# Kernel optimization log

Measured on AMD Instinct MI355X. Metric: run time of the kernel, lower is better.

The kernel has to match this reference:

```python
import jax, jax.numpy as jnp
import numpy as np
from jax.scipy.linalg import expm

B, T, N_IN, N_HID, N_OUT = 8192, 2048, 2, 10, 10


def setup_inputs() -> dict:
    key = jax.random.key(0)
    k0, k1, k2, k3, k4 = jax.random.split(key, 5)
    inputs = jax.random.normal(k0, (B, T, N_IN), dtype=jnp.float32)
    # skew-symmetric seed for the orthogonal recurrent kernel (expm parametrization)
    A = jax.random.normal(k1, (N_HID, N_HID), dtype=jnp.float32) * 0.1
    # input_kernel: nn.Linear(n_inputs, n_hidden, bias=False) -> weight [H, D_in]
    W_in = jax.random.normal(k2, (N_HID, N_IN), dtype=jnp.float32) / np.sqrt(N_IN)
    # modrelu bias, initialized uniform(-0.01, 0.01) as in exprnn
    b_mod = jax.random.uniform(k3, (N_HID,), jnp.float32, -0.01, 0.01)
    # final nn.Linear(n_hidden, n_outputs)
    lin_W = jax.random.normal(k4, (N_OUT, N_HID), dtype=jnp.float32) / np.sqrt(N_HID)
    lin_b = jnp.zeros((N_OUT,), jnp.float32)
    return {"inputs": inputs, "A": A, "W_in": W_in, "b_mod": b_mod,
            "lin_W": lin_W, "lin_b": lin_b}


def _modrelu(z, b):
    # modrelu(z) = sign(z) * relu(|z| + b)
    return jnp.sign(z) * jax.nn.relu(jnp.abs(z) + b)


def reference(inputs, A, W_in, b_mod, lin_W, lin_b):
    # Orthogonal recurrent matrix: Bmat = expm(skew(A)), skew from strict upper triangle
    A_tri = jnp.triu(A, k=1)
    Bmat = expm(A_tri - A_tri.T)  # [H, H], orthogonal
    # Precompute input projections for all timesteps: [B, T, H]
    x_proj = jnp.einsum('btd,hd->bth', inputs, W_in)
    h0 = jnp.zeros((inputs.shape[0], W_in.shape[0]), dtype=inputs.dtype)

    def step(h, x_t):
        h_new = _modrelu(x_t + h @ Bmat, b_mod)
        return h_new, None

    hT, _ = jax.lax.scan(step, h0, jnp.swapaxes(x_proj, 0, 1))  # scan over time
    out = hT @ lin_W.T + lin_b  # [B, n_outputs]
    return out
```

## Files before the change

kernel.cpp:

```cpp
#include <hip/hip_runtime.h>

#define H 10
#define T_LEN 2048
#define BATCH 8192

#define MOVROR(x, K) __int_as_float(__builtin_amdgcn_mov_dpp(                    \
    __float_as_int(x), 0x120 + (K), 0xF, 0xF, true))

__global__ void expm_kernel(const float* __restrict__ A, float* __restrict__ Bout) {
    __shared__ double S[H][H];
    __shared__ double P[H][H];
    __shared__ double E[H][H];
    const int tid = threadIdx.x;
    const int i = tid / H, j = tid % H;
    if (tid < H * H) {
        double a = 0.0;
        if (i < j) a = (double)A[i * H + j];
        else if (i > j) a = -(double)A[j * H + i];
        a *= (1.0 / 256.0);
        S[i][j] = a;
        P[i][j] = a;
        E[i][j] = (i == j ? 1.0 : 0.0) + a;
    }
    __syncthreads();
    for (int k = 2; k <= 16; ++k) {
        double acc = 0.0;
        if (tid < H * H) {
            for (int m = 0; m < H; ++m) acc += P[i][m] * S[m][j];
            acc *= (1.0 / (double)k);
        }
        __syncthreads();
        if (tid < H * H) { P[i][j] = acc; E[i][j] += acc; }
        __syncthreads();
    }
    for (int rr = 0; rr < 8; ++rr) {
        double acc = 0.0;
        if (tid < H * H) {
            for (int m = 0; m < H; ++m) acc += E[i][m] * E[m][j];
        }
        __syncthreads();
        if (tid < H * H) E[i][j] = acc;
        __syncthreads();
    }
    if (tid < H * H) Bout[i * H + j] = (float)E[i][j];
}

__global__ __launch_bounds__(64)
void rnn_kernel(const float* __restrict__ x,
                const float* __restrict__ Bm,
                const float* __restrict__ Win,
                const float* __restrict__ bmod,
                const float* __restrict__ lW,
                const float* __restrict__ lb,
                float* __restrict__ out) {
    const int lane = threadIdx.x;
    const int j    = lane & 15;
    const int row  = lane >> 4;
    const int bb   = blockIdx.x * 4 + row;

    float Brot[16];
#pragma unroll
    for (int k = 0; k < 16; ++k) {
        const int m = (j - k) & 15;
        Brot[k] = (j < H && m < H) ? Bm[m * H + j] : 0.f;
    }
    float w0j = 0.f, w1j = 0.f, bmj = 0.f;
    if (j < H) { w0j = Win[j * 2]; w1j = Win[j * 2 + 1]; bmj = bmod[j]; }

    float h = 0.f;

    const float4* __restrict__ xp4 = (const float4*)(x + (size_t)bb * (T_LEN * 2));
    float4 buf[8];
#pragma unroll
    for (int i = 0; i < 8; ++i) buf[i] = xp4[i];

    for (int t0 = 0; t0 < T_LEN; t0 += 16) {
        float4 c[8];
#pragma unroll
        for (int i = 0; i < 8; ++i) c[i] = buf[i];
        if (t0 + 16 < T_LEN) {
            const int base = (t0 + 16) >> 1;
#pragma unroll
            for (int i = 0; i < 8; ++i) buf[i] = xp4[base + i];
        }

#pragma unroll
        for (int u = 0; u < 16; ++u) {
            const int ii = u >> 1;
            const float x0 = (u & 1) ? c[ii].z : c[ii].x;
            const float x1 = (u & 1) ? c[ii].w : c[ii].y;

            float acc = fmaf(x1, w1j, x0 * w0j);
            acc = fmaf(h, Brot[0], acc);
#define STEPK(K) { const float e_ = MOVROR(h, K); acc = fmaf(e_, Brot[K], acc); }
            STEPK(1)  STEPK(2)  STEPK(3)  STEPK(4)  STEPK(5)
            STEPK(6)  STEPK(7)  STEPK(8)  STEPK(9)  STEPK(10)
            STEPK(11) STEPK(12) STEPK(13) STEPK(14) STEPK(15)
#undef STEPK
            const float s = acc;
            const float r = fmaxf(fabsf(s) + bmj, 0.f);
            h = __builtin_copysignf(r, s);
        }
    }

    float Lrot[16];
#pragma unroll
    for (int k = 0; k < 16; ++k) {
        const int m = (j - k) & 15;
        Lrot[k] = (j < H && m < H) ? lW[j * H + m] : 0.f;
    }
    float acc = (j < H) ? lb[j] : 0.f;
    acc = fmaf(h, Lrot[0], acc);
#define OUTK(K) { const float e_ = MOVROR(h, K); acc = fmaf(e_, Lrot[K], acc); }
    OUTK(1)  OUTK(2)  OUTK(3)  OUTK(4)  OUTK(5)
    OUTK(6)  OUTK(7)  OUTK(8)  OUTK(9)  OUTK(10)
    OUTK(11) OUTK(12) OUTK(13) OUTK(14) OUTK(15)
#undef OUTK
    if (j < H) out[(size_t)bb * H + j] = acc;
}

extern "C" void kernel_launch(void* const* d_in, const int* in_sizes, int n_in,
                              void* d_out, int out_size, void* d_ws, size_t ws_size,
                              hipStream_t stream) {
    const float* inputs = (const float*)d_in[0];
    const float* A      = (const float*)d_in[1];
    const float* W_in   = (const float*)d_in[2];
    const float* b_mod  = (const float*)d_in[3];
    const float* lin_W  = (const float*)d_in[4];
    const float* lin_b  = (const float*)d_in[5];
    float* out = (float*)d_out;
    float* Bmat = (float*)d_ws;

    expm_kernel<<<1, 128, 0, stream>>>(A, Bmat);
    rnn_kernel<<<BATCH / 4, 64, 0, stream>>>(inputs, Bmat, W_in, b_mod,
                                             lin_W, lin_b, out);
}
```

Baseline: 389.5 us.

## Fold DPP row rotations into v_fmac via inline asm and double-buffer input loads

Replaces each separate DPP mov plus FMA with a single v_fmac_f32 carrying a row_ror DPP modifier, written in inline asm. This roughly halves the instruction count on the serial recurrence critical path. Input prefetch now uses two ping-pong register buffers over 32 timesteps, which removes the buffer copy. Launch bounds gain a minimum of 2 blocks. The s_nop before the first DPP op covers the VALU-write-to-DPP-read hazard, but inline asm hides these dependencies from the compiler's hazard tracking and scheduling.

```diff
diff --git a/kernel.cpp b/kernel.cpp
--- a/kernel.cpp
+++ b/kernel.cpp
@@ -6,6 +6,14 @@
 
 #define MOVROR(x, K) __int_as_float(__builtin_amdgcn_mov_dpp(                    \
     __float_as_int(x), 0x120 + (K), 0xF, 0xF, true))
+
+#define STR_(x) #x
+#define FMAC_ROR(acc, hh, bk, K)                                                  \
+    asm("v_fmac_f32 %0, %1, %2 row_ror:" STR_(K) " row_mask:0xf bank_mask:0xf"    \
+        : "+v"(acc) : "v"(hh), "v"(bk))
+#define FMAC_ROR1(acc, hh, bk)                                                    \
+    asm("s_nop 1\n\tv_fmac_f32 %0, %1, %2 row_ror:1 row_mask:0xf bank_mask:0xf"   \
+        : "+v"(acc) : "v"(hh), "v"(bk))
 
 __global__ void expm_kernel(const float* __restrict__ A, float* __restrict__ Bout) {
     __shared__ double S[H][H];
@@ -45,7 +53,47 @@
     if (tid < H * H) Bout[i * H + j] = (float)E[i][j];
 }
 
-__global__ __launch_bounds__(64)
+struct RnnConsts {
+    float w0j, w1j, bmj;
+};
+
+__device__ __forceinline__ void rnn_step(float x0, float x1, float& h,
+                                         const float (&Brot)[16],
+                                         const RnnConsts& cst) {
+    float acc = fmaf(x1, cst.w1j, x0 * cst.w0j);
+    acc = fmaf(h, Brot[0], acc);
+    FMAC_ROR1(acc, h, Brot[1]);
+    FMAC_ROR(acc, h, Brot[2],  2);
+    FMAC_ROR(acc, h, Brot[3],  3);
+    FMAC_ROR(acc, h, Brot[4],  4);
+    FMAC_ROR(acc, h, Brot[5],  5);
+    FMAC_ROR(acc, h, Brot[6],  6);
+    FMAC_ROR(acc, h, Brot[7],  7);
+    FMAC_ROR(acc, h, Brot[8],  8);
+    FMAC_ROR(acc, h, Brot[9],  9);
+    FMAC_ROR(acc, h, Brot[10], 10);
+    FMAC_ROR(acc, h, Brot[11], 11);
+    FMAC_ROR(acc, h, Brot[12], 12);
+    FMAC_ROR(acc, h, Brot[13], 13);
+    FMAC_ROR(acc, h, Brot[14], 14);
+    FMAC_ROR(acc, h, Brot[15], 15);
+    const float r = fmaxf(fabsf(acc) + cst.bmj, 0.f);
+    h = __builtin_copysignf(r, acc);
+}
+
+__device__ __forceinline__ void run16(const float4 (&c)[8], float& h,
+                                      const float (&Brot)[16],
+                                      const RnnConsts& cst) {
+#pragma unroll
+    for (int u = 0; u < 16; ++u) {
+        const int ii = u >> 1;
+        const float x0 = (u & 1) ? c[ii].z : c[ii].x;
+        const float x1 = (u & 1) ? c[ii].w : c[ii].y;
+        rnn_step(x0, x1, h, Brot, cst);
+    }
+}
+
+__global__ __launch_bounds__(64, 2)
 void rnn_kernel(const float* __restrict__ x,
                 const float* __restrict__ Bm,
                 const float* __restrict__ Win,
@@ -64,43 +112,27 @@
         const int m = (j - k) & 15;
         Brot[k] = (j < H && m < H) ? Bm[m * H + j] : 0.f;
     }
-    float w0j = 0.f, w1j = 0.f, bmj = 0.f;
-    if (j < H) { w0j = Win[j * 2]; w1j = Win[j * 2 + 1]; bmj = bmod[j]; }
+    RnnConsts cst = {0.f, 0.f, 0.f};
+    if (j < H) { cst.w0j = Win[j * 2]; cst.w1j = Win[j * 2 + 1]; cst.bmj = bmod[j]; }
 
     float h = 0.f;
 
     const float4* __restrict__ xp4 = (const float4*)(x + (size_t)bb * (T_LEN * 2));
-    float4 buf[8];
+    float4 bA[8], bB[8];
 #pragma unroll
-    for (int i = 0; i < 8; ++i) buf[i] = xp4[i];
+    for (int i = 0; i < 8; ++i) bA[i] = xp4[i];
 
-    for (int t0 = 0; t0 < T_LEN; t0 += 16) {
-        float4 c[8];
+    for (int t0 = 0; t0 < T_LEN; t0 += 32) {
+        const int baseB = (t0 + 16) >> 1;
 #pragma unroll
-        for (int i = 0; i < 8; ++i) c[i] = buf[i];
-        if (t0 + 16 < T_LEN) {
-            const int base = (t0 + 16) >> 1;
+        for (int i = 0; i < 8; ++i) bB[i] = xp4[baseB + i];
+        run16(bA, h, Brot, cst);
+        if (t0 + 32 < T_LEN) {
+            const int baseA = (t0 + 32) >> 1;
 #pragma unroll
-            for (int i = 0; i < 8; ++i) buf[i] = xp4[base + i];
+            for (int i = 0; i < 8; ++i) bA[i] = xp4[baseA + i];
         }
-
-#pragma unroll
-        for (int u = 0; u < 16; ++u) {
-            const int ii = u >> 1;
-            const float x0 = (u & 1) ? c[ii].z : c[ii].x;
-            const float x1 = (u & 1) ? c[ii].w : c[ii].y;
-
-            float acc = fmaf(x1, w1j, x0 * w0j);
-            acc = fmaf(h, Brot[0], acc);
-#define STEPK(K) { const float e_ = MOVROR(h, K); acc = fmaf(e_, Brot[K], acc); }
-            STEPK(1)  STEPK(2)  STEPK(3)  STEPK(4)  STEPK(5)
-            STEPK(6)  STEPK(7)  STEPK(8)  STEPK(9)  STEPK(10)
-            STEPK(11) STEPK(12) STEPK(13) STEPK(14) STEPK(15)
-#undef STEPK
-            const float s = acc;
-            const float r = fmaxf(fabsf(s) + bmj, 0.f);
-            h = __builtin_copysignf(r, s);
-        }
+        run16(bB, h, Brot, cst);
     }
 
     float Lrot[16];
```

New measurement: 345.4 us. 11.3% less time.

## Hand-write RNN recurrence in inline asm with DPP-fused FMAs and split accumulators

Applied to the files above, without the earlier changes.

Replaces the compiled time loop with inline assembly that folds the row-rotate DPP into each v_fmac and splits the 16-term dot product into two interleaved accumulator chains. The two chains are summed before modReLU, which is done with bit masking and v_bfi. Input loads use a four-stage rotating register buffer with manual vmcnt waits to overlap memory with the serial recurrence. This targets per-step latency on the dependent chain, but hard-codes VGPRs v60-v127 and adds launch_bounds occupancy 2, so register pressure may limit other code.

```diff
diff --git a/kernel.cpp b/kernel.cpp
--- a/kernel.cpp
+++ b/kernel.cpp
@@ -6,6 +6,51 @@
 
 #define MOVROR(x, K) __int_as_float(__builtin_amdgcn_mov_dpp(                    \
     __float_as_int(x), 0x120 + (K), 0xF, 0xF, true))
+
+#define STR2(x) #x
+#define VREG(n) "v" STR2(n)
+#define DPP_(K) " row_ror:" STR2(K) " row_mask:0xf bank_mask:0xf\n\t"
+
+#define STEP(X0, X1)                                                \
+    "v_mul_f32 v62, " VREG(X0) ", %[w0]\n\t"                        \
+    "v_fmac_f32 v62, " VREG(X1) ", %[w1]\n\t"                       \
+    "v_fmac_f32 v62, %[h], %[b0]\n\t"                               \
+    "v_mul_f32 v63, %[h], %[b8]" DPP_(8)                            \
+    "v_fmac_f32 v62, %[h], %[b1]" DPP_(1)                           \
+    "v_fmac_f32 v63, %[h], %[b9]" DPP_(9)                           \
+    "v_fmac_f32 v62, %[h], %[b2]" DPP_(2)                           \
+    "v_fmac_f32 v63, %[h], %[b10]" DPP_(10)                         \
+    "v_fmac_f32 v62, %[h], %[b3]" DPP_(3)                           \
+    "v_fmac_f32 v63, %[h], %[b11]" DPP_(11)                         \
+    "v_fmac_f32 v62, %[h], %[b4]" DPP_(4)                           \
+    "v_fmac_f32 v63, %[h], %[b12]" DPP_(12)                         \
+    "v_fmac_f32 v62, %[h], %[b5]" DPP_(5)                           \
+    "v_fmac_f32 v63, %[h], %[b13]" DPP_(13)                         \
+    "v_fmac_f32 v62, %[h], %[b6]" DPP_(6)                           \
+    "v_fmac_f32 v63, %[h], %[b14]" DPP_(14)                         \
+    "v_fmac_f32 v62, %[h], %[b7]" DPP_(7)                           \
+    "v_fmac_f32 v63, %[h], %[b15]" DPP_(15)                         \
+    "v_add_f32 v62, v62, v63\n\t"                                   \
+    "v_and_b32 v63, %[mk], v62\n\t"                                 \
+    "v_add_f32 v63, v63, %[bm]\n\t"                                 \
+    "v_max_f32 v63, 0, v63\n\t"                                     \
+    "v_bfi_b32 %[h], %[mk], v63, v62\n\t"
+
+#define SUBCTL(TAG, LD0, LD1, LD2, LD3)                             \
+    "s_cmp_lt_u32 %[it], 253\n\t"                                   \
+    "s_cbranch_scc0 Lsk" TAG "_%=\n\t"                              \
+    "global_load_dwordx4 " LD0 ", v[60:61], off\n\t"                \
+    "global_load_dwordx4 " LD1 ", v[60:61], off offset:16\n\t"      \
+    "global_load_dwordx4 " LD2 ", v[60:61], off offset:32\n\t"      \
+    "global_load_dwordx4 " LD3 ", v[60:61], off offset:48\n\t"      \
+    "v_add_co_u32 v60, vcc, 64, v60\n\t"                            \
+    "v_addc_co_u32 v61, vcc, 0, v61, vcc\n\t"                       \
+    "s_waitcnt vmcnt(12)\n\t"                                       \
+    "s_branch Ldn" TAG "_%=\n\t"                                    \
+    "Lsk" TAG "_%=:\n\t"                                            \
+    "s_waitcnt vmcnt(0)\n\t"                                        \
+    "Ldn" TAG "_%=:\n\t"                                            \
+    "s_add_i32 %[it], %[it], 1\n\t"
 
 __global__ void expm_kernel(const float* __restrict__ A, float* __restrict__ Bout) {
     __shared__ double S[H][H];
@@ -45,7 +90,7 @@
     if (tid < H * H) Bout[i * H + j] = (float)E[i][j];
 }
 
-__global__ __launch_bounds__(64)
+__global__ __launch_bounds__(64, 2)
 void rnn_kernel(const float* __restrict__ x,
                 const float* __restrict__ Bm,
                 const float* __restrict__ Win,
@@ -58,50 +103,69 @@
     const int row  = lane >> 4;
     const int bb   = blockIdx.x * 4 + row;
 
-    float Brot[16];
+    float Bv[16];
 #pragma unroll
     for (int k = 0; k < 16; ++k) {
         const int m = (j - k) & 15;
-        Brot[k] = (j < H && m < H) ? Bm[m * H + j] : 0.f;
+        Bv[k] = (j < H && m < H) ? Bm[m * H + j] : 0.f;
     }
     float w0j = 0.f, w1j = 0.f, bmj = 0.f;
     if (j < H) { w0j = Win[j * 2]; w1j = Win[j * 2 + 1]; bmj = bmod[j]; }
 
     float h = 0.f;
-
-    const float4* __restrict__ xp4 = (const float4*)(x + (size_t)bb * (T_LEN * 2));
-    float4 buf[8];
-#pragma unroll
-    for (int i = 0; i < 8; ++i) buf[i] = xp4[i];
-
-    for (int t0 = 0; t0 < T_LEN; t0 += 16) {
-        float4 c[8];
-#pragma unroll
-        for (int i = 0; i < 8; ++i) c[i] = buf[i];
-        if (t0 + 16 < T_LEN) {
-            const int base = (t0 + 16) >> 1;
-#pragma unroll
-            for (int i = 0; i < 8; ++i) buf[i] = xp4[base + i];
-        }
-
-#pragma unroll
-        for (int u = 0; u < 16; ++u) {
-            const int ii = u >> 1;
-            const float x0 = (u & 1) ? c[ii].z : c[ii].x;
-            const float x1 = (u & 1) ? c[ii].w : c[ii].y;
-
-            float acc = fmaf(x1, w1j, x0 * w0j);
-            acc = fmaf(h, Brot[0], acc);
-#define STEPK(K) { const float e_ = MOVROR(h, K); acc = fmaf(e_, Brot[K], acc); }
-            STEPK(1)  STEPK(2)  STEPK(3)  STEPK(4)  STEPK(5)
-            STEPK(6)  STEPK(7)  STEPK(8)  STEPK(9)  STEPK(10)
-            STEPK(11) STEPK(12) STEPK(13) STEPK(14) STEPK(15)
-#undef STEPK
-            const float s = acc;
-            const float r = fmaxf(fabsf(s) + bmj, 0.f);
-            h = __builtin_copysignf(r, s);
-        }
-    }
+    int it = 0;
+    const uint64_t addr = (uint64_t)(x + (size_t)bb * (T_LEN * 2));
+    const unsigned alo = (unsigned)addr, ahi = (unsigned)(addr >> 32);
+
+    asm volatile(
+        "v_mov_b32 v60, %[alo]\n\t"
+        "v_mov_b32 v61, %[ahi]\n\t"
+        "global_load_dwordx4 v[64:67],   v[60:61], off\n\t"
+        "global_load_dwordx4 v[68:71],   v[60:61], off offset:16\n\t"
+        "global_load_dwordx4 v[72:75],   v[60:61], off offset:32\n\t"
+        "global_load_dwordx4 v[76:79],   v[60:61], off offset:48\n\t"
+        "global_load_dwordx4 v[80:83],   v[60:61], off offset:64\n\t"
+        "global_load_dwordx4 v[84:87],   v[60:61], off offset:80\n\t"
+        "global_load_dwordx4 v[88:91],   v[60:61], off offset:96\n\t"
+        "global_load_dwordx4 v[92:95],   v[60:61], off offset:112\n\t"
+        "global_load_dwordx4 v[96:99],   v[60:61], off offset:128\n\t"
+        "global_load_dwordx4 v[100:103], v[60:61], off offset:144\n\t"
+        "global_load_dwordx4 v[104:107], v[60:61], off offset:160\n\t"
+        "global_load_dwordx4 v[108:111], v[60:61], off offset:176\n\t"
+        "v_add_co_u32 v60, vcc, 0xc0, v60\n\t"
+        "v_addc_co_u32 v61, vcc, 0, v61, vcc\n\t"
+        "Lmain_%=:\n\t"
+        SUBCTL("0", "v[112:115]", "v[116:119]", "v[120:123]", "v[124:127]")
+        STEP(64, 65)  STEP(66, 67)  STEP(68, 69)  STEP(70, 71)
+        STEP(72, 73)  STEP(74, 75)  STEP(76, 77)  STEP(78, 79)
+        SUBCTL("1", "v[64:67]", "v[68:71]", "v[72:75]", "v[76:79]")
+        STEP(80, 81)  STEP(82, 83)  STEP(84, 85)  STEP(86, 87)
+        STEP(88, 89)  STEP(90, 91)  STEP(92, 93)  STEP(94, 95)
+        SUBCTL("2", "v[80:83]", "v[84:87]", "v[88:91]", "v[92:95]")
+        STEP(96, 97)  STEP(98, 99)  STEP(100, 101) STEP(102, 103)
+        STEP(104, 105) STEP(106, 107) STEP(108, 109) STEP(110, 111)
+        SUBCTL("3", "v[96:99]", "v[100:103]", "v[104:107]", "v[108:111]")
+        STEP(112, 113) STEP(114, 115) STEP(116, 117) STEP(118, 119)
+        STEP(120, 121) STEP(122, 123) STEP(124, 125) STEP(126, 127)
+        "s_cmp_lg_u32 %[it], 256\n\t"
+        "s_cbranch_scc1 Lmain_%=\n\t"
+        : [h] "+v"(h), [it] "+s"(it)
+        : [alo] "v"(alo), [ahi] "v"(ahi),
+          [w0] "v"(w0j), [w1] "v"(w1j), [bm] "v"(bmj),
+          [mk] "s"(0x7fffffffu),
+          [b0] "v"(Bv[0]),  [b1] "v"(Bv[1]),  [b2] "v"(Bv[2]),  [b3] "v"(Bv[3]),
+          [b4] "v"(Bv[4]),  [b5] "v"(Bv[5]),  [b6] "v"(Bv[6]),  [b7] "v"(Bv[7]),
+          [b8] "v"(Bv[8]),  [b9] "v"(Bv[9]),  [b10] "v"(Bv[10]), [b11] "v"(Bv[11]),
+          [b12] "v"(Bv[12]), [b13] "v"(Bv[13]), [b14] "v"(Bv[14]), [b15] "v"(Bv[15])
+        : "memory", "vcc", "scc",
+          "v60", "v61", "v62", "v63", "v64", "v65", "v66", "v67", "v68", "v69",
+          "v70", "v71", "v72", "v73", "v74", "v75", "v76", "v77", "v78", "v79",
+          "v80", "v81", "v82", "v83", "v84", "v85", "v86", "v87", "v88", "v89",
+          "v90", "v91", "v92", "v93", "v94", "v95", "v96", "v97", "v98", "v99",
+          "v100", "v101", "v102", "v103", "v104", "v105", "v106", "v107",
+          "v108", "v109", "v110", "v111", "v112", "v113", "v114", "v115",
+          "v116", "v117", "v118", "v119", "v120", "v121", "v122", "v123",
+          "v124", "v125", "v126", "v127");
 
     float Lrot[16];
 #pragma unroll
```

Result: faster. 333.9 us (-14.3%).

## Move recurrent matvec onto MFMA with split-fp16 and fuse expm into RNN kernel

Applied to the files above, without the earlier changes.

Replaces the per-lane DPP rotate-and-FMA recurrence with 16x16x16 fp16 MFMA instructions, handling 16 batch rows per wavefront instead of 4. To keep near-fp32 accuracy, both the recurrent matrix and the hidden state are split into hi/lo fp16 parts, which costs three MFMAs per step. The separate expm kernel is removed and every block recomputes the matrix exponential in shared memory, dropping one launch but repeating that setup work in all 512 blocks. Each step now sits on a serial MFMA latency chain, and the hi/lo split still loses some precision compared with full fp32.

```diff
diff --git a/kernel.cpp b/kernel.cpp
--- a/kernel.cpp
+++ b/kernel.cpp
@@ -4,119 +4,159 @@
 #define T_LEN 2048
 #define BATCH 8192
 
-#define MOVROR(x, K) __int_as_float(__builtin_amdgcn_mov_dpp(                    \
-    __float_as_int(x), 0x120 + (K), 0xF, 0xF, true))
+typedef _Float16 f16x4 __attribute__((ext_vector_type(4)));
+typedef float f32x4 __attribute__((ext_vector_type(4)));
 
-__global__ void expm_kernel(const float* __restrict__ A, float* __restrict__ Bout) {
-    __shared__ double S[H][H];
-    __shared__ double P[H][H];
-    __shared__ double E[H][H];
-    const int tid = threadIdx.x;
-    const int i = tid / H, j = tid % H;
-    if (tid < H * H) {
-        double a = 0.0;
-        if (i < j) a = (double)A[i * H + j];
-        else if (i > j) a = -(double)A[j * H + i];
-        a *= (1.0 / 256.0);
-        S[i][j] = a;
-        P[i][j] = a;
-        E[i][j] = (i == j ? 1.0 : 0.0) + a;
-    }
-    __syncthreads();
-    for (int k = 2; k <= 16; ++k) {
-        double acc = 0.0;
-        if (tid < H * H) {
-            for (int m = 0; m < H; ++m) acc += P[i][m] * S[m][j];
-            acc *= (1.0 / (double)k);
-        }
-        __syncthreads();
-        if (tid < H * H) { P[i][j] = acc; E[i][j] += acc; }
-        __syncthreads();
-    }
-    for (int rr = 0; rr < 8; ++rr) {
-        double acc = 0.0;
-        if (tid < H * H) {
-            for (int m = 0; m < H; ++m) acc += E[i][m] * E[m][j];
-        }
-        __syncthreads();
-        if (tid < H * H) E[i][j] = acc;
-        __syncthreads();
-    }
-    if (tid < H * H) Bout[i * H + j] = (float)E[i][j];
+__device__ __forceinline__ f32x4 mfma16(f16x4 a, f16x4 b, f32x4 c) {
+#if __has_builtin(__builtin_amdgcn_mfma_f32_16x16x16f16)
+    return __builtin_amdgcn_mfma_f32_16x16x16f16(a, b, c, 0, 0, 0);
+#else
+    f32x4 d;
+    asm("v_mfma_f32_16x16x16_f16 %0, %1, %2, %3"
+        : "=v"(d) : "v"(a), "v"(b), "v"(c));
+    return d;
+#endif
 }
 
 __global__ __launch_bounds__(64)
 void rnn_kernel(const float* __restrict__ x,
-                const float* __restrict__ Bm,
+                const float* __restrict__ A,
                 const float* __restrict__ Win,
                 const float* __restrict__ bmod,
                 const float* __restrict__ lW,
                 const float* __restrict__ lb,
                 float* __restrict__ out) {
-    const int lane = threadIdx.x;
-    const int j    = lane & 15;
-    const int row  = lane >> 4;
-    const int bb   = blockIdx.x * 4 + row;
+    __shared__ double S[H][H];
+    __shared__ double Pm[H][H];
+    __shared__ double E[H][H];
+    __shared__ float hsh[16][16];
+    const int tid = threadIdx.x;
 
-    float Brot[16];
-#pragma unroll
-    for (int k = 0; k < 16; ++k) {
-        const int m = (j - k) & 15;
-        Brot[k] = (j < H && m < H) ? Bm[m * H + j] : 0.f;
-    }
-    float w0j = 0.f, w1j = 0.f, bmj = 0.f;
-    if (j < H) { w0j = Win[j * 2]; w1j = Win[j * 2 + 1]; bmj = bmod[j]; }
-
-    float h = 0.f;
-
-    const float4* __restrict__ xp4 = (const float4*)(x + (size_t)bb * (T_LEN * 2));
-    float4 buf[8];
-#pragma unroll
-    for (int i = 0; i < 8; ++i) buf[i] = xp4[i];
-
-    for (int t0 = 0; t0 < T_LEN; t0 += 16) {
-        float4 c[8];
-#pragma unroll
-        for (int i = 0; i < 8; ++i) c[i] = buf[i];
-        if (t0 + 16 < T_LEN) {
-            const int base = (t0 + 16) >> 1;
-#pragma unroll
-            for (int i = 0; i < 8; ++i) buf[i] = xp4[base + i];
+    {
+        const int e0 = tid, e1 = tid + 64;
+        const int i0 = e0 / H, j0 = e0 % H;
+        const int i1 = e1 / H, j1 = e1 % H;
+        const bool v1 = (e1 < H * H);
+        double a0 = 0.0;
+        if (i0 < j0) a0 = (double)A[i0 * H + j0];
+        else if (i0 > j0) a0 = -(double)A[j0 * H + i0];
+        a0 *= (1.0 / 256.0);
+        S[i0][j0] = a0; Pm[i0][j0] = a0;
+        E[i0][j0] = (i0 == j0 ? 1.0 : 0.0) + a0;
+        if (v1) {
+            double a1 = 0.0;
+            if (i1 < j1) a1 = (double)A[i1 * H + j1];
+            else if (i1 > j1) a1 = -(double)A[j1 * H + i1];
+            a1 *= (1.0 / 256.0);
+            S[i1][j1] = a1; Pm[i1][j1] = a1;
+            E[i1][j1] = (i1 == j1 ? 1.0 : 0.0) + a1;
         }
-
-#pragma unroll
-        for (int u = 0; u < 16; ++u) {
-            const int ii = u >> 1;
-            const float x0 = (u & 1) ? c[ii].z : c[ii].x;
-            const float x1 = (u & 1) ? c[ii].w : c[ii].y;
-
-            float acc = fmaf(x1, w1j, x0 * w0j);
-            acc = fmaf(h, Brot[0], acc);
-#define STEPK(K) { const float e_ = MOVROR(h, K); acc = fmaf(e_, Brot[K], acc); }
-            STEPK(1)  STEPK(2)  STEPK(3)  STEPK(4)  STEPK(5)
-            STEPK(6)  STEPK(7)  STEPK(8)  STEPK(9)  STEPK(10)
-            STEPK(11) STEPK(12) STEPK(13) STEPK(14) STEPK(15)
-#undef STEPK
-            const float s = acc;
-            const float r = fmaxf(fabsf(s) + bmj, 0.f);
-            h = __builtin_copysignf(r, s);
+        __syncthreads();
+        for (int k = 2; k <= 16; ++k) {
+            double t0 = 0.0, t1 = 0.0;
+            for (int m = 0; m < H; ++m) t0 += Pm[i0][m] * S[m][j0];
+            t0 *= (1.0 / (double)k);
+            if (v1) {
+                for (int m = 0; m < H; ++m) t1 += Pm[i1][m] * S[m][j1];
+                t1 *= (1.0 / (double)k);
+            }
+            __syncthreads();
+            Pm[i0][j0] = t0; E[i0][j0] += t0;
+            if (v1) { Pm[i1][j1] = t1; E[i1][j1] += t1; }
+            __syncthreads();
+        }
+        for (int rr = 0; rr < 8; ++rr) {
+            double t0 = 0.0, t1 = 0.0;
+            for (int m = 0; m < H; ++m) t0 += E[i0][m] * E[m][j0];
+            if (v1) {
+                for (int m = 0; m < H; ++m) t1 += E[i1][m] * E[m][j1];
+            }
+            __syncthreads();
+            E[i0][j0] = t0;
+            if (v1) E[i1][j1] = t1;
+            __syncthreads();
         }
     }
 
-    float Lrot[16];
+    const int l15  = tid & 15;
+    const int rrow = tid >> 4;
+    const int bb   = blockIdx.x * 16 + l15;
+
+    f16x4 a_hi, a_lo;
 #pragma unroll
-    for (int k = 0; k < 16; ++k) {
-        const int m = (j - k) & 15;
-        Lrot[k] = (j < H && m < H) ? lW[j * H + m] : 0.f;
+    for (int s = 0; s < 4; ++s) {
+        const int m = rrow * 4 + s;
+        float av = (m < H && l15 < H) ? (float)E[m][l15] : 0.f;
+        _Float16 ah = (_Float16)av;
+        a_hi[s] = ah;
+        a_lo[s] = (_Float16)(av - (float)ah);
     }
-    float acc = (j < H) ? lb[j] : 0.f;
-    acc = fmaf(h, Lrot[0], acc);
-#define OUTK(K) { const float e_ = MOVROR(h, K); acc = fmaf(e_, Lrot[K], acc); }
-    OUTK(1)  OUTK(2)  OUTK(3)  OUTK(4)  OUTK(5)
-    OUTK(6)  OUTK(7)  OUTK(8)  OUTK(9)  OUTK(10)
-    OUTK(11) OUTK(12) OUTK(13) OUTK(14) OUTK(15)
-#undef OUTK
-    if (j < H) out[(size_t)bb * H + j] = acc;
+    float w0v[4], w1v[4], bmv[4];
+#pragma unroll
+    for (int s = 0; s < 4; ++s) {
+        const int j4 = rrow * 4 + s;
+        w0v[s] = (j4 < H) ? Win[j4 * 2]     : 0.f;
+        w1v[s] = (j4 < H) ? Win[j4 * 2 + 1] : 0.f;
+        bmv[s] = (j4 < H) ? bmod[j4]        : 0.f;
+    }
+
+    f16x4 hhi = {};
+    f16x4 hlo = {};
+    f32x4 hf  = {};
+
+    const float4* __restrict__ xp4 = (const float4*)(x + (size_t)bb * (T_LEN * 2));
+    float4 cur[4], nxt[4];
+#pragma unroll
+    for (int i = 0; i < 4; ++i) cur[i] = xp4[i];
+
+    for (int t0 = 0; t0 < T_LEN; t0 += 8) {
+        if (t0 + 8 < T_LEN) {
+            const int base = (t0 + 8) >> 1;
+#pragma unroll
+            for (int i = 0; i < 4; ++i) nxt[i] = xp4[base + i];
+        }
+#pragma unroll
+        for (int u = 0; u < 8; ++u) {
+            const int ii = u >> 1;
+            const float x0 = (u & 1) ? cur[ii].z : cur[ii].x;
+            const float x1 = (u & 1) ? cur[ii].w : cur[ii].y;
+
+            f32x4 c;
+#pragma unroll
+            for (int s = 0; s < 4; ++s)
+                c[s] = fmaf(x1, w1v[s], x0 * w0v[s]);
+
+            f32x4 d = mfma16(a_hi, hhi, c);
+            d = mfma16(a_lo, hhi, d);
+            d = mfma16(a_hi, hlo, d);
+
+#pragma unroll
+            for (int s = 0; s < 4; ++s) {
+                const float sv = d[s];
+                const float r  = fmaxf(fabsf(sv) + bmv[s], 0.f);
+                const float h  = __builtin_copysignf(r, sv);
+                hf[s] = h;
+                const _Float16 hh = (_Float16)h;
+                hhi[s] = hh;
+                hlo[s] = (_Float16)(h - (float)hh);
+            }
+        }
+#pragma unroll
+        for (int i = 0; i < 4; ++i) cur[i] = nxt[i];
+    }
+
+    __syncthreads();
+#pragma unroll
+    for (int s = 0; s < 4; ++s) hsh[rrow * 4 + s][l15] = hf[s];
+    __syncthreads();
+    for (int i = tid; i < 16 * H; i += 64) {
+        const int b = i / H, comp = i - b * H;
+        float acc = lb[comp];
+#pragma unroll
+        for (int m = 0; m < H; ++m)
+            acc = fmaf(hsh[m][b], lW[comp * H + m], acc);
+        out[(size_t)(blockIdx.x * 16 + b) * H + comp] = acc;
+    }
 }
 
 extern "C" void kernel_launch(void* const* d_in, const int* in_sizes, int n_in,
@@ -129,9 +169,8 @@
     const float* lin_W  = (const float*)d_in[4];
     const float* lin_b  = (const float*)d_in[5];
     float* out = (float*)d_out;
-    float* Bmat = (float*)d_ws;
+    (void)d_ws; (void)ws_size;
 
-    expm_kernel<<<1, 128, 0, stream>>>(A, Bmat);
-    rnn_kernel<<<BATCH / 4, 64, 0, stream>>>(inputs, Bmat, W_in, b_mod,
-                                             lin_W, lin_b, out);
+    rnn_kernel<<<BATCH / 16, 64, 0, stream>>>(inputs, A, W_in, b_mod,
+                                              lin_W, lin_b, out);
 }
```

New measurement: 458.5 us. +17.7%, slower.
